# Kernel optimization log

Hardware: AMD Instinct MI355X
Metric: run time of the kernel (lower is better)

Reference implementation:

```python
import jax, jax.numpy as jnp
import numpy as np

H, B = 2, 64          # num_head, batch
LT, LI, LQ = 384, 128, 24
D = 768               # input_dim == hidden_dim
K = 384               # key_dim
V = 384               # value_dim
DK, DV = H * K, H * V # fused key / value dims (768, 768)


def _layer_norm(x, g, b, eps=1e-5):
    mu = x.mean(-1, keepdims=True)
    var = ((x - mu) ** 2).mean(-1, keepdims=True)
    return (x - mu) / jnp.sqrt(var + eps) * g + b


def _masked_softmax(w):
    # softmax over last axis treating -inf as masked; fully-masked rows -> all zeros
    # (faithful to torch: softmax then masked_fill_(isnan, 0))
    valid = jnp.isfinite(w)
    wmax = jnp.max(jnp.where(valid, w, -3e38), axis=-1, keepdims=True)
    e = jnp.where(valid, jnp.exp(w - wmax), 0.0)
    s = jnp.sum(e, axis=-1, keepdims=True)
    return e / jnp.where(s > 0, s, 1.0)


def _forward(text, images, query, ln_gamma, ln_beta,
             Wsq, bsq, Wiq, biq, Wsk, bsk, Wik, bik, Wsv, bsv, Wiv, biv,
             Wkp, bkp, Wvp, bvp,
             text_lengths, image_lengths, query_lengths):
    Bq, Lt, _ = text.shape
    Li = images.shape[1]
    L = Lt + Li
    tn = _layer_norm(text, ln_gamma, ln_beta)
    im = _layer_norm(images, ln_gamma, ln_beta)

    def proj(Wt, bt, Wi, bi):
        a = jnp.einsum('btd,hdk->hbtk', tn, Wt) + bt[:, None, None, :]
        c = jnp.einsum('bid,hdk->hbik', im, Wi) + bi[:, None, None, :]
        return jnp.concatenate([a, c], axis=2)  # [H,B,L,K or V]

    q = proj(Wsq, bsq, Wiq, biq)
    k = proj(Wsk, bsk, Wik, bik)
    v = proj(Wsv, bsv, Wiv, biv)

    # pad mask: True = padded position (torch mask==1 -> masked_fill 0)
    pad = jnp.concatenate([
        jnp.arange(Lt)[None, :] >= text_lengths[:, None],
        jnp.arange(Li)[None, :] >= image_lengths[:, None]], axis=1)  # [B,L]
    pm = pad[None, :, :, None]
    q = jnp.where(pm, 0.0, q)
    k = jnp.where(pm, 0.0, k)
    v = jnp.where(pm, 0.0, v)

    # SelfAttention per head: zero-dot-product masking + diagonal exclusion
    w = jnp.einsum('hbqd,hbkd->hbqk', q, k)
    w = jnp.where(w == 0.0, -jnp.inf, w)
    w = jnp.where(jnp.eye(L, dtype=bool)[None, None], -jnp.inf, w)
    p = _masked_softmax(w)
    attn = jnp.einsum('hbqk,hbkd->hbqd', p, v)          # [H,B,L,V]
    album = jnp.transpose(attn, (1, 2, 0, 3)).reshape(Bq, L, H * V)  # head-concat

    keys = album @ Wkp + bkp   # [B,L,DK]
    vals = album @ Wvp + bvp   # [B,L,DV]

    # FVTA: mask query / keys / values, zero-score -> -inf, softmax, nan -> 0
    padq = jnp.arange(query.shape[1])[None, :] >= query_lengths[:, None]
    qf = jnp.where(padq[..., None], 0.0, query)
    keys = jnp.where(pad[..., None], 0.0, keys)
    vals = jnp.where(pad[..., None], 0.0, vals)
    w2 = jnp.einsum('bqd,bkd->bqk', qf, keys)
    w2 = jnp.where(w2 == 0.0, -jnp.inf, w2)
    p2 = _masked_softmax(w2)
    return jnp.einsum('bqk,bkv->bqv', p2, vals).mean(axis=1)  # [B,DV]


def setup_inputs() -> dict:
    key = jax.random.key(0)
    ks = jax.random.split(key, 24)
    s = 0.02
    return {
        'text':   jax.random.normal(ks[0], (B, LT, D), jnp.float32),
        'images': jax.random.normal(ks[1], (B, LI, D), jnp.float32),
        'query':  jax.random.normal(ks[2], (B, LQ, DK), jnp.float32),
        'ln_gamma': jnp.ones((D,), jnp.float32),
        'ln_beta':  jnp.zeros((D,), jnp.float32),
        'Wsq': jax.random.normal(ks[3], (H, D, K), jnp.float32) * s,
        'bsq': jnp.zeros((H, K), jnp.float32),
        'Wiq': jax.random.normal(ks[4], (H, D, K), jnp.float32) * s,
        'biq': jnp.zeros((H, K), jnp.float32),
        'Wsk': jax.random.normal(ks[5], (H, D, K), jnp.float32) * s,
        'bsk': jnp.zeros((H, K), jnp.float32),
        'Wik': jax.random.normal(ks[6], (H, D, K), jnp.float32) * s,
        'bik': jnp.zeros((H, K), jnp.float32),
        'Wsv': jax.random.normal(ks[7], (H, D, V), jnp.float32) * s,
        'bsv': jnp.zeros((H, V), jnp.float32),
        'Wiv': jax.random.normal(ks[8], (H, D, V), jnp.float32) * s,
        'biv': jnp.zeros((H, V), jnp.float32),
        'Wkp': jax.random.normal(ks[9], (DV, DK), jnp.float32) * s,
        'bkp': jnp.zeros((DK,), jnp.float32),
        'Wvp': jax.random.normal(ks[10], (DV, DV), jnp.float32) * s,
        'bvp': jnp.zeros((DV,), jnp.float32),
        'text_lengths':  jax.random.randint(ks[11], (B,), 1, LT + 1),
        'image_lengths': jax.random.randint(ks[12], (B,), 1, LI + 1),
        'query_lengths': jax.random.randint(ks[13], (B,), 1, LQ + 1),
    }


def reference(text, images, query, ln_gamma, ln_beta,
              Wsq, bsq, Wiq, biq, Wsk, bsk, Wik, bik, Wsv, bsv, Wiv, biv,
              Wkp, bkp, Wvp, bvp,
              text_lengths, image_lengths, query_lengths):
    return _forward(text, images, query, ln_gamma, ln_beta,
                    Wsq, bsq, Wiq, biq, Wsk, bsk, Wik, bik, Wsv, bsv, Wiv, biv,
                    Wkp, bkp, Wvp, bvp,
                    text_lengths, image_lengths, query_lengths)
```

## Files before the change

kernel.cpp:

```cpp
#include <hip/hip_runtime.h>
#include <hip/hip_bf16.h>

typedef _Float16 h16;
typedef _Float16 h16x8 __attribute__((ext_vector_type(8)));
typedef _Float16 h16x4 __attribute__((ext_vector_type(4)));
typedef float    f32x4 __attribute__((ext_vector_type(4)));

#define MFMA(a,b,c) __builtin_amdgcn_mfma_f32_16x16x32_f16((a),(b),(c),0,0,0)


typedef __attribute__((address_space(1))) const void gas_void;
typedef __attribute__((address_space(3))) void las_void;
__device__ __forceinline__ void gld16(void* l, const void* g) {
  __builtin_amdgcn_global_load_lds((gas_void*)g, (las_void*)l, 16, 0, 0);
}

__global__ __launch_bounds__(256) void k_diag(float* out, int n, float val) {
  int i = blockIdx.x * 256 + threadIdx.x;
  if (i < n) out[i] = val;
}

__global__ __launch_bounds__(256) void k_prep(
    const float* __restrict__ Wsq, const float* __restrict__ Wiq,
    const float* __restrict__ Wsk, const float* __restrict__ Wik,
    const float* __restrict__ Wsv, const float* __restrict__ Wiv,
    const float* __restrict__ Wkp, const float* __restrict__ Wvp,
    h16* __restrict__ wb,
    const float* __restrict__ text, const float* __restrict__ images,
    const float* __restrict__ g, const float* __restrict__ be,
    h16* __restrict__ xn,
    const int* __restrict__ tlen, const int* __restrict__ ilen)
{
  const size_t WSZ = 589824;
  int bid = blockIdx.x;
  if (bid < 4608) {
    const float* src; h16* dst;
    int cols, cx, cy;
    if (bid < 3456) {
      int z = bid / 288, rem = bid % 288;
      cx = rem % 12; cy = rem / 12;
      int w = z >> 1, m = z & 1;
      const float* s6[6] = {Wsq, Wiq, Wsk, Wik, Wsv, Wiv};
      src = s6[w] + (size_t)m * 768 * 384;
      dst = wb + (size_t)w * WSZ + (size_t)m * 384 * 768;
      cols = 384;
    } else {
      int u2 = bid - 3456;
      int z = u2 / 576, rem = u2 % 576;
      cx = rem % 24; cy = rem / 24;
      src = (z == 0) ? Wkp : Wvp;
      dst = wb + (size_t)(6 + z) * WSZ;
      cols = 768;
    }
    __shared__ float tile[32][33];
    int d0 = cy * 32, c0 = cx * 32;
    int tx = threadIdx.x & 31, ty = threadIdx.x >> 5;
    #pragma unroll
    for (int i = 0; i < 32; i += 8)
      tile[ty+i][tx] = src[(size_t)(d0+ty+i)*cols + c0 + tx];
    __syncthreads();
    #pragma unroll
    for (int i = 0; i < 32; i += 8)
      dst[(size_t)(c0+ty+i)*768 + d0 + tx] = (h16)tile[tx][ty+i];
    return;
  }
  int row = bid - 4608;
  int b = row >> 9, l = row & 511;
  bool pad = (l < 384) ? (l >= tlen[b]) : ((l-384) >= ilen[b]);
  if (pad) return;
  const float* src = (l < 384) ? (text + ((size_t)b*384 + l)*768)
                               : (images + ((size_t)b*128 + (l-384))*768);
  int t = threadIdx.x;
  float x0 = src[t], x1 = src[t+256], x2 = src[t+512];
  __shared__ float red[8];
  float s = x0 + x1 + x2;
  #pragma unroll
  for (int m = 32; m; m >>= 1) s += __shfl_xor(s, m);
  int wid = t >> 6;
  if ((t & 63) == 0) red[wid] = s;
  __syncthreads();
  float mu = (red[0]+red[1]+red[2]+red[3]) * (1.0f/768.0f);
  float d0 = x0-mu, d1 = x1-mu, d2 = x2-mu;
  float v = d0*d0 + d1*d1 + d2*d2;
  #pragma unroll
  for (int m = 32; m; m >>= 1) v += __shfl_xor(v, m);
  if ((t & 63) == 0) red[4+wid] = v;
  __syncthreads();
  float var = (red[4]+red[5]+red[6]+red[7]) * (1.0f/768.0f);
  float rstd = rsqrtf(var + 1e-5f);
  h16* dst = xn + (size_t)row * 768;
  dst[t]     = (h16)(d0*rstd*g[t]     + be[t]);
  dst[t+256] = (h16)(d1*rstd*g[t+256] + be[t+256]);
  dst[t+512] = (h16)(d2*rstd*g[t+512] + be[t+512]);
}

__global__ __launch_bounds__(256) void k_lnstat(
    const float* __restrict__ text, const float* __restrict__ images,
    float* __restrict__ muv, float* __restrict__ rsd)
{
  int row = blockIdx.x;
  int b = row >> 9, l = row & 511;
  const float* src = (l < 384) ? (text + ((size_t)b*384 + l)*768)
                               : (images + ((size_t)b*128 + (l-384))*768);
  int t = threadIdx.x;
  float x0 = src[t], x1 = src[t+256], x2 = src[t+512];
  __shared__ float red[8];
  float s = x0 + x1 + x2;
  #pragma unroll
  for (int m = 32; m; m >>= 1) s += __shfl_xor(s, m);
  int wid = t >> 6;
  if ((t & 63) == 0) red[wid] = s;
  __syncthreads();
  float mu = (red[0]+red[1]+red[2]+red[3]) * (1.0f/768.0f);
  float d0 = x0-mu, d1 = x1-mu, d2 = x2-mu;
  float v = d0*d0 + d1*d1 + d2*d2;
  #pragma unroll
  for (int m = 32; m; m >>= 1) v += __shfl_xor(v, m);
  if ((t & 63) == 0) red[4+wid] = v;
  __syncthreads();
  if (t == 0) {
    float var = (red[4]+red[5]+red[6]+red[7]) * (1.0f/768.0f);
    muv[row] = mu;
    rsd[row] = rsqrtf(var + 1e-5f);
  }
}

__global__ __launch_bounds__(256) void k_wprep_all(
    const float* __restrict__ Wsq, const float* __restrict__ Wiq,
    const float* __restrict__ Wsk, const float* __restrict__ Wik,
    const float* __restrict__ Wsv, const float* __restrict__ Wiv,
    const float* __restrict__ Wkp, const float* __restrict__ Wvp,
    h16* __restrict__ wb)
{
  const size_t WSZ = 589824;
  int z = blockIdx.z;
  const float* src; h16* dst;
  int cols;
  if (z < 12) {
    if (blockIdx.x >= 12) return;
    int w = z >> 1, m = z & 1;
    const float* s6[6] = {Wsq, Wiq, Wsk, Wik, Wsv, Wiv};
    src = s6[w] + (size_t)m * 768 * 384;
    dst = wb + (size_t)w * WSZ + (size_t)m * 384 * 768;
    cols = 384;
  } else {
    src = (z == 12) ? Wkp : Wvp;
    dst = wb + (size_t)(6 + (z - 12)) * WSZ;
    cols = 768;
  }
  __shared__ float tile[32][33];
  int d0 = blockIdx.y * 32;
  int c0 = blockIdx.x * 32;
  int tx = threadIdx.x & 31, ty = threadIdx.x >> 5;
  #pragma unroll
  for (int i = 0; i < 32; i += 8)
    tile[ty+i][tx] = src[(size_t)(d0+ty+i)*cols + c0 + tx];
  __syncthreads();
  #pragma unroll
  for (int i = 0; i < 32; i += 8)
    dst[(size_t)(c0+ty+i)*768 + d0 + tx] = (h16)tile[tx][ty+i];
}

#define HOFF ((size_t)64*512*384)

template<int AMODE>
__global__ __launch_bounds__(256) void k_gemmf2(
    const h16* __restrict__ Asrc, const h16* __restrict__ wb,
    const float* __restrict__ bsq, const float* __restrict__ biq,
    const float* __restrict__ bsk, const float* __restrict__ bik,
    const float* __restrict__ bsv, const float* __restrict__ biv,
    const float* __restrict__ bkp, const float* __restrict__ bvp,
    h16* __restrict__ O0, h16* __restrict__ O1, h16* __restrict__ O2,
    const int* __restrict__ tlen, const int* __restrict__ ilen)
{
  constexpr int NT = (AMODE == 0) ? 18 : 12;
  __shared__ __align__(16) h16 SM[32768];
  h16* As0 = SM;
  h16* Bs0 = SM + 16384;
  const size_t WSZ = 589824;
  int bid = blockIdx.x;
  int xcd = bid & 7, slot = bid >> 3;
  int mt = xcd * 32 + slot / NT;
  int nt = slot % NT;
  int m0 = mt << 7;
  int b = m0 >> 9, l0 = m0 & 511;
  int TL = tlen[b], IL = ilen[b];
  bool skiptile = (l0 < 384) && (TL <= l0);
  int gc0 = nt << 7;
  int widx = gc0 / 768;
  int ncol0 = gc0 % 768;
  bool isimg = (l0 >= 384);

  const h16* BT;
  const float* bias;
  if constexpr (AMODE == 0) {
    BT = wb + ((size_t)(2*widx) + (isimg ? 1 : 0)) * WSZ;
    const float* bt6[6] = {bsq, biq, bsk, bik, bsv, biv};
    bias = bt6[2*widx + (isimg ? 1 : 0)];
  } else {
    BT = wb + (size_t)(6 + widx) * WSZ;
    bias = widx ? bvp : bkp;
  }

  int t = threadIdx.x;
  int lane = t & 63, wid = t >> 6;
  int wm = wid >> 1, wn = wid & 1;
  int lg = lane >> 4, li = lane & 15;

  f32x4 acc44[4][4] = {};

  if (!skiptile) {
    const h16* pA[4]; const h16* pB[4];
    h16* dA[4]; h16* dB[4];
    #pragma unroll
    for (int h = 0; h < 4; ++h) {
      int ci = h*256 + t;
      int row = ci >> 3;
      int cs = (ci & 7) ^ (row & 7);
      if constexpr (AMODE == 0)
        pA[h] = Asrc + (size_t)(m0 + row)*768 + cs*8;
      else
        pA[h] = Asrc + ((size_t)b*512 + l0 + row)*384 + cs*8;
      pB[h] = BT + (size_t)(ncol0 + row)*768 + cs*8;
      dA[h] = &As0[(h*256 + wid*64)*8];
      dB[h] = &Bs0[(h*256 + wid*64)*8];
    }
    const char* baA = (const char*)As0 + (wm*64 + li)*128;
    const char* baB = (const char*)Bs0 + (wn*64 + li)*128;
    int x0 = (lg ^ (li & 7)) << 4;

    #pragma unroll
    for (int h = 0; h < 4; ++h) {
      gld16(dA[h], pA[h]);
      gld16(dB[h], pB[h]);
    }
    __syncthreads();

    #pragma unroll
    for (int kk = 0; kk < 12; ++kk) {
      const int cur = kk & 1;
      if (kk < 11) {
        int ktE = (kk + 1) * 64;
        size_t aoff = (size_t)ktE;
        if constexpr (AMODE == 2) { if (ktE >= 384) aoff += HOFF - 384; }
        #pragma unroll
        for (int h = 0; h < 4; ++h) {
          gld16(dA[h] + (cur^1)*8192, pA[h] + aoff);
          gld16(dB[h] + (cur^1)*8192, pB[h] + ktE);
        }
      }
      const char* cA = baA + cur*16384;
      const char* cB = baB + cur*16384;
      #pragma unroll
      for (int ks = 0; ks < 2; ++ks) {
        int xo = x0 ^ (ks << 6);
        h16x8 af[4], bf[4];
        #pragma unroll
        for (int i = 0; i < 4; ++i) {
          af[i] = *(const h16x8*)(cA + i*2048 + xo);
          bf[i] = *(const h16x8*)(cB + i*2048 + xo);
        }
        #pragma unroll
        for (int i = 0; i < 4; ++i)
          #pragma unroll
          for (int j = 0; j < 4; ++j)
            acc44[i][j] = MFMA(af[i], bf[j], acc44[i][j]);
      }
      __syncthreads();
    }
  }

  constexpr int PITCH = 136;
  bool vroute = (AMODE == 0) ? (widx == 2) : (widx == 1);
  h16* dout = vroute ? ((AMODE == 0) ? O2 : O1)
                     : ((AMODE == 0) ? (widx == 0 ? O0 : O1) : O0);
  #pragma unroll
  for (int i = 0; i < 4; ++i)
    #pragma unroll
    for (int j = 0; j < 4; ++j) {
      int rowL = wm*64 + i*16 + lg*4;
      int colL = wn*64 + j*16 + li;
      float bv = bias[ncol0 + colL];
      #pragma unroll
      for (int r = 0; r < 4; ++r) {
        int l = l0 + rowL + r;
        float v = acc44[i][j][r] + bv;
        bool pad = (l < 384) ? (l >= TL) : ((l-384) >= IL);
        if (pad) v = 0.0f;
        if (vroute) SM[colL*PITCH + rowL + r] = (h16)v;
        else        SM[(rowL + r)*PITCH + colL] = (h16)v;
      }
    }
  __syncthreads();
  int hh = (AMODE == 0 && ncol0 >= 384) ? 1 : 0;
  int kkb = ncol0 - hh*384;
  #pragma unroll
  for (int q = 0; q < 8; ++q) {
    int row = q*16 + (t >> 4);
    int c0 = (t & 15) * 8;
    h16x8 val = *(const h16x8*)&SM[row*PITCH + c0];
    size_t oi;
    if (vroute) {
      if constexpr (AMODE == 0)
        oi = (((size_t)(hh*64 + b))*384 + kkb + row)*512 + l0 + c0;
      else
        oi = ((size_t)b*768 + ncol0 + row)*512 + l0 + c0;
    } else {
      int l = l0 + row;
      if constexpr (AMODE == 0)
        oi = (((size_t)(hh*64 + b))*512 + l)*384 + kkb + c0;
      else
        oi = ((size_t)b*512 + l)*768 + ncol0 + c0;
    }
    *(uint4*)&dout[oi] = *(uint4*)&val;
  }
}

#define LDSKg 72
__global__ __launch_bounds__(256) void k_gemmf_fb(
    const float* __restrict__ Atext, const float* __restrict__ Aimg,
    const float* __restrict__ muv, const float* __restrict__ rsd,
    const float* __restrict__ gam, const float* __restrict__ bet,
    const h16* __restrict__ wb,
    const float* __restrict__ bsq, const float* __restrict__ biq,
    const float* __restrict__ bsk, const float* __restrict__ bik,
    const float* __restrict__ bsv, const float* __restrict__ biv,
    h16* __restrict__ O0, h16* __restrict__ O1, h16* __restrict__ O2,
    const int* __restrict__ tlen, const int* __restrict__ ilen)
{
  constexpr int NT = 18;
  __shared__ __align__(16) h16 As[128*LDSKg];
  __shared__ __align__(16) h16 Bs[128*LDSKg];
  const size_t WSZ = 589824;
  int bid = blockIdx.x;
  int xcd = bid & 7, slot = bid >> 3;
  int mt = xcd * 32 + slot / NT;
  int nt = slot % NT;
  int m0 = mt << 7;
  int b = m0 >> 9, l0 = m0 & 511;
  int TL = tlen[b], IL = ilen[b];
  bool skiptile = (l0 < 384) && (TL <= l0);
  int gc0 = nt << 7;
  int widx = gc0 / 768;
  int ncol0 = gc0 % 768;
  bool isimg = (l0 >= 384);
  const h16* BT = wb + ((size_t)(2*widx) + (isimg ? 1 : 0)) * WSZ;
  const float* bt6[6] = {bsq, biq, bsk, bik, bsv, biv};
  const float* bias = bt6[2*widx + (isimg ? 1 : 0)];

  int t = threadIdx.x;
  int lane = t & 63, wid = t >> 6;
  int wm = wid >> 1, wn = wid & 1;
  int lg = lane >> 4, li = lane & 15;
  int sr = t >> 3, sc8 = (t & 7) * 8;
  f32x4 acc[4][4] = {};
  if (!skiptile) {
    const float* af32[4];
    float amu[4], ars[4];
    const h16* brow[4];
    #pragma unroll
    for (int half = 0; half < 4; ++half) {
      int r = sr + half*32;
      int l = l0 + r;
      af32[half] = (l < 384) ? (Atext + ((size_t)b*384 + l)*768)
                             : (Aimg  + ((size_t)b*128 + (l-384))*768);
      amu[half] = muv[m0 + r]; ars[half] = rsd[m0 + r];
      brow[half] = BT + (size_t)(ncol0 + r)*768;
    }
    for (int kt = 0; kt < 768; kt += 64) {
      int d = kt + sc8;
      f32x4 g0 = *(const f32x4*)&gam[d], g1 = *(const f32x4*)&gam[d+4];
      f32x4 e0 = *(const f32x4*)&bet[d], e1 = *(const f32x4*)&bet[d+4];
      #pragma unroll
      for (int half = 0; half < 4; ++half) {
        int r = sr + half*32;
        f32x4 x0 = *(const f32x4*)&af32[half][d];
        f32x4 x1 = *(const f32x4*)&af32[half][d+4];
        float mu = amu[half], rs = ars[half];
        h16x8 o;
        #pragma unroll
        for (int j = 0; j < 4; ++j) o[j]   = (h16)((x0[j]-mu)*rs*g0[j] + e0[j]);
        #pragma unroll
        for (int j = 0; j < 4; ++j) o[4+j] = (h16)((x1[j]-mu)*rs*g1[j] + e1[j]);
        *(h16x8*)&As[r*LDSKg + sc8] = o;
        *(uint4*)&Bs[r*LDSKg + sc8] = *(const uint4*)&brow[half][d];
      }
      __syncthreads();
      #pragma unroll
      for (int ks = 0; ks < 2; ++ks) {
        int kc = ks*32 + lg*8;
        h16x8 af[4], bf[4];
        #pragma unroll
        for (int i = 0; i < 4; ++i) {
          af[i] = *(const h16x8*)&As[(wm*64 + i*16 + li)*LDSKg + kc];
          bf[i] = *(const h16x8*)&Bs[(wn*64 + i*16 + li)*LDSKg + kc];
        }
        #pragma unroll
        for (int i = 0; i < 4; ++i)
          #pragma unroll
          for (int j = 0; j < 4; ++j)
            acc[i][j] = MFMA(af[i], bf[j], acc[i][j]);
      }
      __syncthreads();
    }
  }
  bool vroute = (widx == 2);
  h16* dsc = (widx == 0 ? O0 : O1);
  #pragma unroll
  for (int i = 0; i < 4; ++i)
    #pragma unroll
    for (int j = 0; j < 4; ++j) {
      int colL = wn*64 + j*16 + li;
      int col_in = ncol0 + colL;
      float bv = bias[col_in];
      int lb = l0 + wm*64 + i*16 + lg*4;
      int hh = (col_in >= 384) ? 1 : 0;
      int kk = col_in - hh*384;
      if (vroute) {
        h16x4 pk;
        #pragma unroll
        for (int r = 0; r < 4; ++r) {
          int l = lb + r;
          float v = acc[i][j][r] + bv;
          bool pad = (l < 384) ? (l >= TL) : ((l-384) >= IL);
          pk[r] = (h16)(pad ? 0.0f : v);
        }
        size_t oi = (((size_t)(hh*64 + b))*384 + kk)*512 + lb;
        *(h16x4*)&O2[oi] = pk;
      } else {
        #pragma unroll
        for (int r = 0; r < 4; ++r) {
          int l = lb + r;
          float v = acc[i][j][r] + bv;
          bool pad = (l < 384) ? (l >= TL) : ((l-384) >= IL);
          if (pad) v = 0.0f;
          size_t oi = (((size_t)(hh*64 + b))*512 + l)*384 + kk;
          dsc[oi] = (h16)v;
        }
      }
    }
}

__global__ __launch_bounds__(256) void k_attn1(
    h16* Qb, const h16* __restrict__ Kb, const h16* __restrict__ Vt,
    const int* __restrict__ tlen, const int* __restrict__ ilen)
{
  __shared__ __align__(16) float S[32*516];
  __shared__ float rowscale[32];
  int bid = blockIdx.x;
  int xcd = bid & 7, slot = bid >> 3;
  int hb = (slot >> 4) * 8 + xcd;
  int q0 = (slot & 15) * 32;
  int b = hb & 63;
  int TL = tlen[b], IL = ilen[b];
  h16* Qp = Qb + (size_t)hb * 512 * 384;
  const h16* Kp = Kb + (size_t)hb * 512 * 384;
  const h16* Vp = Vt + (size_t)hb * 384 * 512;
  int t = threadIdx.x, lane = t & 63, w = t >> 6;
  int lg = lane >> 4, li = lane & 15;

  bool qskip = (q0 < 384) ? (TL <= q0) : (IL <= q0 - 384);
  if (qskip) {
    h16x8 z = {};
    for (int c = t; c < 1536; c += 256) {
      int row = c / 48, v8 = (c % 48) * 8;
      *(h16x8*)&Qp[(size_t)(q0+row)*384 + v8] = z;
    }
    return;
  }

  h16x8 aq[2][12];
  #pragma unroll
  for (int m = 0; m < 2; ++m)
    #pragma unroll
    for (int ks = 0; ks < 12; ++ks)
      aq[m][ks] = *(const h16x8*)&Qp[(size_t)(q0 + m*16 + li)*384 + ks*32 + lg*8];

  int kbase = w * 128;
  int LIMw = (w < 3) ? TL : (384 + IL);
  int nvf = (LIMw - kbase + 15) >> 4;
  nvf = nvf < 0 ? 0 : (nvf > 8 ? 8 : nvf);
  for (int nf = 0; nf < nvf; ++nf) {
    int kcol = kbase + nf*16;
    f32x4 acc0 = {0,0,0,0}, acc1 = {0,0,0,0};
    #pragma unroll
    for (int ks = 0; ks < 12; ++ks) {
      h16x8 bk = *(const h16x8*)&Kp[(size_t)(kcol + li)*384 + ks*32 + lg*8];
      acc0 = MFMA(aq[0][ks], bk, acc0);
      acc1 = MFMA(aq[1][ks], bk, acc1);
    }
    #pragma unroll
    for (int r = 0; r < 4; ++r) {
      int c = kcol + li;
      int row0 = lg*4 + r;
      float v0 = acc0[r];
      if (v0 == 0.0f || (q0 + row0) == c) v0 = -__builtin_inff();
      S[row0*516 + c] = v0;
      int row1 = 16 + lg*4 + r;
      float v1 = acc1[r];
      if (v1 == 0.0f || (q0 + row1) == c) v1 = -__builtin_inff();
      S[row1*516 + c] = v1;
    }
  }
  for (int nf = nvf; nf < 8; ++nf) {
    int c = kbase + nf*16 + li;
    #pragma unroll
    for (int r = 0; r < 4; ++r) {
      S[(lg*4 + r)*516 + c] = -__builtin_inff();
      S[(16 + lg*4 + r)*516 + c] = -__builtin_inff();
    }
  }
  __syncthreads();
  {
    int row = t >> 3, ci = t & 7;
    float mx = -3e38f;
    for (int j = 0; j < 64; ++j) mx = fmaxf(mx, S[row*516 + ci + j*8]);
    mx = fmaxf(mx, __shfl_xor(mx, 1));
    mx = fmaxf(mx, __shfl_xor(mx, 2));
    mx = fmaxf(mx, __shfl_xor(mx, 4));
    float sum = 0.0f;
    for (int j = 0; j < 64; ++j) {
      float e = __expf(S[row*516 + ci + j*8] - mx);
      S[row*516 + ci + j*8] = e;
      sum += e;
    }
    sum += __shfl_xor(sum, 1);
    sum += __shfl_xor(sum, 2);
    sum += __shfl_xor(sum, 4);
    if (ci == 0) rowscale[row] = 1.0f / (sum > 0.0f ? sum : 1.0f);
  }
  __syncthreads();
  f32x4 oacc[2][6] = {};
  int v0w = w * 96;
  auto pv = [&](int kt) {
    int k0 = kt * 32;
    h16x8 bv[6];
    #pragma unroll
    for (int n = 0; n < 6; ++n)
      bv[n] = *(const h16x8*)&Vp[(size_t)(v0w + n*16 + li)*512 + k0 + lg*8];
    #pragma unroll
    for (int m = 0; m < 2; ++m) {
      int row = m*16 + li;
      f32x4 p0 = *(const f32x4*)&S[row*516 + k0 + lg*8];
      f32x4 p1 = *(const f32x4*)&S[row*516 + k0 + lg*8 + 4];
      h16x8 pa;
      pa[0]=(h16)p0[0]; pa[1]=(h16)p0[1]; pa[2]=(h16)p0[2]; pa[3]=(h16)p0[3];
      pa[4]=(h16)p1[0]; pa[5]=(h16)p1[1]; pa[6]=(h16)p1[2]; pa[7]=(h16)p1[3];
      #pragma unroll
      for (int n = 0; n < 6; ++n)
        oacc[m][n] = MFMA(pa, bv[n], oacc[m][n]);
    }
  };
  int n1 = (TL + 31) >> 5; n1 = n1 > 12 ? 12 : n1;
  int n2 = (IL + 31) >> 5; n2 = n2 > 4 ? 4 : n2;
  for (int kt = 0; kt < n1; ++kt) pv(kt);
  for (int kt = 12; kt < 12 + n2; ++kt) pv(kt);
  #pragma unroll
  for (int m = 0; m < 2; ++m)
    #pragma unroll
    for (int n = 0; n < 6; ++n)
      #pragma unroll
      for (int r = 0; r < 4; ++r) {
        int row = m*16 + lg*4 + r;
        int col = v0w + n*16 + li;
        Qp[(size_t)(q0 + row)*384 + col] = (h16)(oacc[m][n][r] * rowscale[row]);
      }
}

__global__ __launch_bounds__(256) void k_attn2(
    const float* __restrict__ query, const h16* __restrict__ keys,
    const h16* __restrict__ valsT, const int* __restrict__ qlen,
    const int* __restrict__ tlen, const int* __restrict__ ilen,
    float* __restrict__ out)
{
  __shared__ __align__(16) float S[32*516];
  __shared__ __align__(16) h16 UB[32*776];
  __shared__ float rowscale[32];
  int bid = blockIdx.x;
  int b = bid >> 1, vh = bid & 1;
  const float* Qp = query + (size_t)b*24*768;
  const h16* Kp = keys + (size_t)b*512*768;
  const h16* Vp = valsT + (size_t)b*768*512;
  int t = threadIdx.x, lane = t & 63, w = t >> 6;
  int lg = lane >> 4, li = lane & 15;
  int ql = qlen[b];
  int TL = tlen[b], IL = ilen[b];
  for (int c = t; c < 3072; c += 256) {
    int row = c / 96, vv = (c % 96) * 8;
    h16x8 a = {};
    if (row < 24 && row < ql) {
      f32x4 f0 = *(const f32x4*)&Qp[(size_t)row*768 + vv];
      f32x4 f1 = *(const f32x4*)&Qp[(size_t)row*768 + vv + 4];
      a[0]=(h16)f0[0]; a[1]=(h16)f0[1]; a[2]=(h16)f0[2]; a[3]=(h16)f0[3];
      a[4]=(h16)f1[0]; a[5]=(h16)f1[1]; a[6]=(h16)f1[2]; a[7]=(h16)f1[3];
    }
    *(h16x8*)&UB[row*776 + vv] = a;
  }
  __syncthreads();
  int kbase = w * 128;
  int LIMw = (w < 3) ? TL : (384 + IL);
  int nvf = (LIMw - kbase + 15) >> 4;
  nvf = nvf < 0 ? 0 : (nvf > 8 ? 8 : nvf);
  for (int nf = 0; nf < nvf; ++nf) {
    int kcol = kbase + nf*16;
    f32x4 acc0 = {0,0,0,0}, acc1 = {0,0,0,0};
    #pragma unroll
    for (int ks = 0; ks < 24; ++ks) {
      h16x8 a0 = *(const h16x8*)&UB[(li)*776      + ks*32 + lg*8];
      h16x8 a1 = *(const h16x8*)&UB[(16 + li)*776 + ks*32 + lg*8];
      h16x8 bk = *(const h16x8*)&Kp[(size_t)(kcol + li)*768 + ks*32 + lg*8];
      acc0 = MFMA(a0, bk, acc0);
      acc1 = MFMA(a1, bk, acc1);
    }
    #pragma unroll
    for (int r = 0; r < 4; ++r) {
      int c = kcol + li;
      float v0 = acc0[r];
      if (v0 == 0.0f) v0 = -__builtin_inff();
      S[(lg*4 + r)*516 + c] = v0;
      float v1 = acc1[r];
      if (v1 == 0.0f) v1 = -__builtin_inff();
      S[(16 + lg*4 + r)*516 + c] = v1;
    }
  }
  for (int nf = nvf; nf < 8; ++nf) {
    int c = kbase + nf*16 + li;
    #pragma unroll
    for (int r = 0; r < 4; ++r) {
      S[(lg*4 + r)*516 + c] = -__builtin_inff();
      S[(16 + lg*4 + r)*516 + c] = -__builtin_inff();
    }
  }
  __syncthreads();
  {
    int row = t >> 3, ci = t & 7;
    float mx = -3e38f;
    for (int j = 0; j < 64; ++j) mx = fmaxf(mx, S[row*516 + ci + j*8]);
    mx = fmaxf(mx, __shfl_xor(mx, 1));
    mx = fmaxf(mx, __shfl_xor(mx, 2));
    mx = fmaxf(mx, __shfl_xor(mx, 4));
    float sum = 0.0f;
    for (int j = 0; j < 64; ++j) {
      float e = __expf(S[row*516 + ci + j*8] - mx);
      S[row*516 + ci + j*8] = e;
      sum += e;
    }
    sum += __shfl_xor(sum, 1);
    sum += __shfl_xor(sum, 2);
    sum += __shfl_xor(sum, 4);
    if (ci == 0) rowscale[row] = 1.0f / (sum > 0.0f ? sum : 1.0f);
  }
  __syncthreads();
  int n1 = (TL + 31) >> 5; n1 = n1 > 12 ? 12 : n1;
  int n2 = (IL + 31) >> 5; n2 = n2 > 4 ? 4 : n2;
  {
    f32x4 oacc[2][6] = {};
    auto pv = [&](int kt) {
      int k0 = kt * 32;
      h16x8 bv[6];
      #pragma unroll
      for (int n = 0; n < 6; ++n)
        bv[n] = *(const h16x8*)&Vp[(size_t)(vh*384 + w*96 + n*16 + li)*512 + k0 + lg*8];
      #pragma unroll
      for (int m = 0; m < 2; ++m) {
        int row = m*16 + li;
        f32x4 p0 = *(const f32x4*)&S[row*516 + k0 + lg*8];
        f32x4 p1 = *(const f32x4*)&S[row*516 + k0 + lg*8 + 4];
        h16x8 pa;
        pa[0]=(h16)p0[0]; pa[1]=(h16)p0[1]; pa[2]=(h16)p0[2]; pa[3]=(h16)p0[3];
        pa[4]=(h16)p1[0]; pa[5]=(h16)p1[1]; pa[6]=(h16)p1[2]; pa[7]=(h16)p1[3];
        #pragma unroll
        for (int n = 0; n < 6; ++n)
          oacc[m][n] = MFMA(pa, bv[n], oacc[m][n]);
      }
    };
    for (int kt = 0; kt < n1; ++kt) pv(kt);
    for (int kt = 12; kt < 12 + n2; ++kt) pv(kt);
    #pragma unroll
    for (int n = 0; n < 6; ++n) {
      float cs = 0.0f;
      #pragma unroll
      for (int m = 0; m < 2; ++m)
        #pragma unroll
        for (int r = 0; r < 4; ++r)
          cs += oacc[m][n][r] * rowscale[m*16 + lg*4 + r];
      cs += __shfl_xor(cs, 16);
      cs += __shfl_xor(cs, 32);
      if (lg == 0) out[(size_t)b*768 + vh*384 + w*96 + n*16 + li] = cs * (1.0f/24.0f);
    }
  }
}

extern "C" void kernel_launch(void* const* d_in, const int* in_sizes, int n_in,
                              void* d_out, int out_size, void* d_ws, size_t ws_size,
                              hipStream_t stream)
{
  (void)in_sizes; (void)n_in;
  const float* text  = (const float*)d_in[0];
  const float* images= (const float*)d_in[1];
  const float* query = (const float*)d_in[2];
  const float* ln_g  = (const float*)d_in[3];
  const float* ln_b  = (const float*)d_in[4];
  const float* Wsq = (const float*)d_in[5];
  const float* bsq = (const float*)d_in[6];
  const float* Wiq = (const float*)d_in[7];
  const float* biq = (const float*)d_in[8];
  const float* Wsk = (const float*)d_in[9];
  const float* bsk = (const float*)d_in[10];
  const float* Wik = (const float*)d_in[11];
  const float* bik = (const float*)d_in[12];
  const float* Wsv = (const float*)d_in[13];
  const float* bsv = (const float*)d_in[14];
  const float* Wiv = (const float*)d_in[15];
  const float* biv = (const float*)d_in[16];
  const float* Wkp = (const float*)d_in[17];
  const float* bkp = (const float*)d_in[18];
  const float* Wvp = (const float*)d_in[19];
  const float* bvp = (const float*)d_in[20];
  const int* tlen = (const int*)d_in[21];
  const int* ilen = (const int*)d_in[22];
  const int* qlen = (const int*)d_in[23];

  const size_t NEED1 = 160694272;
  const size_t NEED2 = NEED1 + 50331648;
  if (ws_size < NEED1) {
    k_diag<<<dim3((out_size+255)/256), dim3(256), 0, stream>>>((float*)d_out, out_size, 1.0e6f);
    return;
  }
  float* muv = (float*)d_ws;
  float* rsd = muv + 32768;
  h16* wb = (h16*)((char*)d_ws + 262144);
  const size_t WSZ = 589824;
  const size_t TSZ = (size_t)32768*768;
  h16* Qb = wb + 8*WSZ;
  h16* Kb = Qb + TSZ;
  h16* Vb = Kb + TSZ;
  h16* XNb = (h16*)((char*)d_ws + NEED1);

  dim3 blk(256);

  if (ws_size >= NEED2) {
    k_prep<<<dim3(4608 + 32768), blk, 0, stream>>>(
        Wsq, Wiq, Wsk, Wik, Wsv, Wiv, Wkp, Wvp, wb,
        text, images, ln_g, ln_b, XNb, tlen, ilen);
    k_gemmf2<0><<<dim3(4608), blk, 0, stream>>>(XNb, wb,
        bsq, biq, bsk, bik, bsv, biv, bkp, bvp, Qb, Kb, Vb, tlen, ilen);
  } else {
    k_wprep_all<<<dim3(24,24,14), blk, 0, stream>>>(Wsq, Wiq, Wsk, Wik, Wsv, Wiv, Wkp, Wvp, wb);
    k_lnstat<<<dim3(32768), blk, 0, stream>>>(text, images, muv, rsd);
    k_gemmf_fb<<<dim3(4608), blk, 0, stream>>>(text, images, muv, rsd,
        ln_g, ln_b, wb, bsq, biq, bsk, bik, bsv, biv, Qb, Kb, Vb, tlen, ilen);
  }

  k_attn1<<<dim3(2048), blk, 0, stream>>>(Qb, Kb, Vb, tlen, ilen);

  k_gemmf2<2><<<dim3(3072), blk, 0, stream>>>(Qb, wb,
      bsq, biq, bsk, bik, bsv, biv, bkp, bvp, Kb, Vb, nullptr, tlen, ilen);

  k_attn2<<<dim3(128), blk, 0, stream>>>(query, Kb, Vb, qlen, tlen, ilen, (float*)d_out);
}
```

Before: 435.0 us.

## Store Q/K/V in k-blocked layout and vectorize softmax LDS passes

The projection GEMM epilogue now writes Q, K and V, plus the second-stage keys and values, in a blocked layout with 32-wide k chunks. This makes each MFMA fragment load in the attention kernels a contiguous 16-byte read from a compact block instead of a long-stride row access. The attention output goes to a separate album buffer (reusing the layernorm scratch) rather than overwriting Q in place. The softmax max/exp passes in both attention kernels now use f32x4 LDS reads, and the unused fallback path (k_lnstat, k_wprep_all, k_gemmf_fb) is removed, so the kernel now requires the larger workspace.

```diff
diff --git a/kernel.cpp b/kernel.cpp
--- a/kernel.cpp
+++ b/kernel.cpp
@@ -94,73 +94,6 @@
   dst[t+512] = (h16)(d2*rstd*g[t+512] + be[t+512]);
 }
 
-__global__ __launch_bounds__(256) void k_lnstat(
-    const float* __restrict__ text, const float* __restrict__ images,
-    float* __restrict__ muv, float* __restrict__ rsd)
-{
-  int row = blockIdx.x;
-  int b = row >> 9, l = row & 511;
-  const float* src = (l < 384) ? (text + ((size_t)b*384 + l)*768)
-                               : (images + ((size_t)b*128 + (l-384))*768);
-  int t = threadIdx.x;
-  float x0 = src[t], x1 = src[t+256], x2 = src[t+512];
-  __shared__ float red[8];
-  float s = x0 + x1 + x2;
-  #pragma unroll
-  for (int m = 32; m; m >>= 1) s += __shfl_xor(s, m);
-  int wid = t >> 6;
-  if ((t & 63) == 0) red[wid] = s;
-  __syncthreads();
-  float mu = (red[0]+red[1]+red[2]+red[3]) * (1.0f/768.0f);
-  float d0 = x0-mu, d1 = x1-mu, d2 = x2-mu;
-  float v = d0*d0 + d1*d1 + d2*d2;
-  #pragma unroll
-  for (int m = 32; m; m >>= 1) v += __shfl_xor(v, m);
-  if ((t & 63) == 0) red[4+wid] = v;
-  __syncthreads();
-  if (t == 0) {
-    float var = (red[4]+red[5]+red[6]+red[7]) * (1.0f/768.0f);
-    muv[row] = mu;
-    rsd[row] = rsqrtf(var + 1e-5f);
-  }
-}
-
-__global__ __launch_bounds__(256) void k_wprep_all(
-    const float* __restrict__ Wsq, const float* __restrict__ Wiq,
-    const float* __restrict__ Wsk, const float* __restrict__ Wik,
-    const float* __restrict__ Wsv, const float* __restrict__ Wiv,
-    const float* __restrict__ Wkp, const float* __restrict__ Wvp,
-    h16* __restrict__ wb)
-{
-  const size_t WSZ = 589824;
-  int z = blockIdx.z;
-  const float* src; h16* dst;
-  int cols;
-  if (z < 12) {
-    if (blockIdx.x >= 12) return;
-    int w = z >> 1, m = z & 1;
-    const float* s6[6] = {Wsq, Wiq, Wsk, Wik, Wsv, Wiv};
-    src = s6[w] + (size_t)m * 768 * 384;
-    dst = wb + (size_t)w * WSZ + (size_t)m * 384 * 768;
-    cols = 384;
-  } else {
-    src = (z == 12) ? Wkp : Wvp;
-    dst = wb + (size_t)(6 + (z - 12)) * WSZ;
-    cols = 768;
-  }
-  __shared__ float tile[32][33];
-  int d0 = blockIdx.y * 32;
-  int c0 = blockIdx.x * 32;
-  int tx = threadIdx.x & 31, ty = threadIdx.x >> 5;
-  #pragma unroll
-  for (int i = 0; i < 32; i += 8)
-    tile[ty+i][tx] = src[(size_t)(d0+ty+i)*cols + c0 + tx];
-  __syncthreads();
-  #pragma unroll
-  for (int i = 0; i < 32; i += 8)
-    dst[(size_t)(c0+ty+i)*768 + d0 + tx] = (h16)tile[tx][ty+i];
-}
-
 #define HOFF ((size_t)64*512*384)
 
 template<int AMODE>
@@ -301,148 +234,29 @@
     h16x8 val = *(const h16x8*)&SM[row*PITCH + c0];
     size_t oi;
     if (vroute) {
+      int l = l0 + c0;
+      int kt = l >> 5, k32 = l & 31;
       if constexpr (AMODE == 0)
-        oi = (((size_t)(hh*64 + b))*384 + kkb + row)*512 + l0 + c0;
+        oi = (size_t)(hh*64 + b)*196608 + (size_t)kt*12288 + (size_t)(kkb + row)*32 + k32;
       else
-        oi = ((size_t)b*768 + ncol0 + row)*512 + l0 + c0;
+        oi = (size_t)b*393216 + (size_t)kt*24576 + (size_t)(ncol0 + row)*32 + k32;
     } else {
       int l = l0 + row;
-      if constexpr (AMODE == 0)
-        oi = (((size_t)(hh*64 + b))*512 + l)*384 + kkb + c0;
-      else
-        oi = ((size_t)b*512 + l)*768 + ncol0 + c0;
+      if constexpr (AMODE == 0) {
+        int kk = kkb + c0;
+        oi = (size_t)(hh*64 + b)*196608 + (size_t)(kk >> 5)*16384 + (size_t)l*32 + (kk & 31);
+      } else {
+        int col = ncol0 + c0;
+        oi = (size_t)b*393216 + (size_t)(col >> 5)*16384 + (size_t)l*32 + (col & 31);
+      }
     }
     *(uint4*)&dout[oi] = *(uint4*)&val;
   }
 }
 
-#define LDSKg 72
-__global__ __launch_bounds__(256) void k_gemmf_fb(
-    const float* __restrict__ Atext, const float* __restrict__ Aimg,
-    const float* __restrict__ muv, const float* __restrict__ rsd,
-    const float* __restrict__ gam, const float* __restrict__ bet,
-    const h16* __restrict__ wb,
-    const float* __restrict__ bsq, const float* __restrict__ biq,
-    const float* __restrict__ bsk, const float* __restrict__ bik,
-    const float* __restrict__ bsv, const float* __restrict__ biv,
-    h16* __restrict__ O0, h16* __restrict__ O1, h16* __restrict__ O2,
-    const int* __restrict__ tlen, const int* __restrict__ ilen)
-{
-  constexpr int NT = 18;
-  __shared__ __align__(16) h16 As[128*LDSKg];
-  __shared__ __align__(16) h16 Bs[128*LDSKg];
-  const size_t WSZ = 589824;
-  int bid = blockIdx.x;
-  int xcd = bid & 7, slot = bid >> 3;
-  int mt = xcd * 32 + slot / NT;
-  int nt = slot % NT;
-  int m0 = mt << 7;
-  int b = m0 >> 9, l0 = m0 & 511;
-  int TL = tlen[b], IL = ilen[b];
-  bool skiptile = (l0 < 384) && (TL <= l0);
-  int gc0 = nt << 7;
-  int widx = gc0 / 768;
-  int ncol0 = gc0 % 768;
-  bool isimg = (l0 >= 384);
-  const h16* BT = wb + ((size_t)(2*widx) + (isimg ? 1 : 0)) * WSZ;
-  const float* bt6[6] = {bsq, biq, bsk, bik, bsv, biv};
-  const float* bias = bt6[2*widx + (isimg ? 1 : 0)];
-
-  int t = threadIdx.x;
-  int lane = t & 63, wid = t >> 6;
-  int wm = wid >> 1, wn = wid & 1;
-  int lg = lane >> 4, li = lane & 15;
-  int sr = t >> 3, sc8 = (t & 7) * 8;
-  f32x4 acc[4][4] = {};
-  if (!skiptile) {
-    const float* af32[4];
-    float amu[4], ars[4];
-    const h16* brow[4];
-    #pragma unroll
-    for (int half = 0; half < 4; ++half) {
-      int r = sr + half*32;
-      int l = l0 + r;
-      af32[half] = (l < 384) ? (Atext + ((size_t)b*384 + l)*768)
-                             : (Aimg  + ((size_t)b*128 + (l-384))*768);
-      amu[half] = muv[m0 + r]; ars[half] = rsd[m0 + r];
-      brow[half] = BT + (size_t)(ncol0 + r)*768;
-    }
-    for (int kt = 0; kt < 768; kt += 64) {
-      int d = kt + sc8;
-      f32x4 g0 = *(const f32x4*)&gam[d], g1 = *(const f32x4*)&gam[d+4];
-      f32x4 e0 = *(const f32x4*)&bet[d], e1 = *(const f32x4*)&bet[d+4];
-      #pragma unroll
-      for (int half = 0; half < 4; ++half) {
-        int r = sr + half*32;
-        f32x4 x0 = *(const f32x4*)&af32[half][d];
-        f32x4 x1 = *(const f32x4*)&af32[half][d+4];
-        float mu = amu[half], rs = ars[half];
-        h16x8 o;
-        #pragma unroll
-        for (int j = 0; j < 4; ++j) o[j]   = (h16)((x0[j]-mu)*rs*g0[j] + e0[j]);
-        #pragma unroll
-        for (int j = 0; j < 4; ++j) o[4+j] = (h16)((x1[j]-mu)*rs*g1[j] + e1[j]);
-        *(h16x8*)&As[r*LDSKg + sc8] = o;
-        *(uint4*)&Bs[r*LDSKg + sc8] = *(const uint4*)&brow[half][d];
-      }
-      __syncthreads();
-      #pragma unroll
-      for (int ks = 0; ks < 2; ++ks) {
-        int kc = ks*32 + lg*8;
-        h16x8 af[4], bf[4];
-        #pragma unroll
-        for (int i = 0; i < 4; ++i) {
-          af[i] = *(const h16x8*)&As[(wm*64 + i*16 + li)*LDSKg + kc];
-          bf[i] = *(const h16x8*)&Bs[(wn*64 + i*16 + li)*LDSKg + kc];
-        }
-        #pragma unroll
-        for (int i = 0; i < 4; ++i)
-          #pragma unroll
-          for (int j = 0; j < 4; ++j)
-            acc[i][j] = MFMA(af[i], bf[j], acc[i][j]);
-      }
-      __syncthreads();
-    }
-  }
-  bool vroute = (widx == 2);
-  h16* dsc = (widx == 0 ? O0 : O1);
-  #pragma unroll
-  for (int i = 0; i < 4; ++i)
-    #pragma unroll
-    for (int j = 0; j < 4; ++j) {
-      int colL = wn*64 + j*16 + li;
-      int col_in = ncol0 + colL;
-      float bv = bias[col_in];
-      int lb = l0 + wm*64 + i*16 + lg*4;
-      int hh = (col_in >= 384) ? 1 : 0;
-      int kk = col_in - hh*384;
-      if (vroute) {
-        h16x4 pk;
-        #pragma unroll
-        for (int r = 0; r < 4; ++r) {
-          int l = lb + r;
-          float v = acc[i][j][r] + bv;
-          bool pad = (l < 384) ? (l >= TL) : ((l-384) >= IL);
-          pk[r] = (h16)(pad ? 0.0f : v);
-        }
-        size_t oi = (((size_t)(hh*64 + b))*384 + kk)*512 + lb;
-        *(h16x4*)&O2[oi] = pk;
-      } else {
-        #pragma unroll
-        for (int r = 0; r < 4; ++r) {
-          int l = lb + r;
-          float v = acc[i][j][r] + bv;
-          bool pad = (l < 384) ? (l >= TL) : ((l-384) >= IL);
-          if (pad) v = 0.0f;
-          size_t oi = (((size_t)(hh*64 + b))*512 + l)*384 + kk;
-          dsc[oi] = (h16)v;
-        }
-      }
-    }
-}
-
 __global__ __launch_bounds__(256) void k_attn1(
-    h16* Qb, const h16* __restrict__ Kb, const h16* __restrict__ Vt,
+    const h16* __restrict__ Qt, const h16* __restrict__ Kt,
+    const h16* __restrict__ Vt, h16* __restrict__ album,
     const int* __restrict__ tlen, const int* __restrict__ ilen)
 {
   __shared__ __align__(16) float S[32*516];
@@ -453,9 +267,10 @@
   int q0 = (slot & 15) * 32;
   int b = hb & 63;
   int TL = tlen[b], IL = ilen[b];
-  h16* Qp = Qb + (size_t)hb * 512 * 384;
-  const h16* Kp = Kb + (size_t)hb * 512 * 384;
-  const h16* Vp = Vt + (size_t)hb * 384 * 512;
+  const h16* Qp = Qt + (size_t)hb * 196608;
+  const h16* Kp = Kt + (size_t)hb * 196608;
+  const h16* Vp = Vt + (size_t)hb * 196608;
+  h16* Ap = album + (size_t)hb * 196608;
   int t = threadIdx.x, lane = t & 63, w = t >> 6;
   int lg = lane >> 4, li = lane & 15;
 
@@ -464,7 +279,7 @@
     h16x8 z = {};
     for (int c = t; c < 1536; c += 256) {
       int row = c / 48, v8 = (c % 48) * 8;
-      *(h16x8*)&Qp[(size_t)(q0+row)*384 + v8] = z;
+      *(h16x8*)&Ap[(size_t)(q0+row)*384 + v8] = z;
     }
     return;
   }
@@ -474,7 +289,7 @@
   for (int m = 0; m < 2; ++m)
     #pragma unroll
     for (int ks = 0; ks < 12; ++ks)
-      aq[m][ks] = *(const h16x8*)&Qp[(size_t)(q0 + m*16 + li)*384 + ks*32 + lg*8];
+      aq[m][ks] = *(const h16x8*)&Qp[(size_t)ks*16384 + (q0 + m*16 + li)*32 + lg*8];
 
   int kbase = w * 128;
   int LIMw = (w < 3) ? TL : (384 + IL);
@@ -485,7 +300,7 @@
     f32x4 acc0 = {0,0,0,0}, acc1 = {0,0,0,0};
     #pragma unroll
     for (int ks = 0; ks < 12; ++ks) {
-      h16x8 bk = *(const h16x8*)&Kp[(size_t)(kcol + li)*384 + ks*32 + lg*8];
+      h16x8 bk = *(const h16x8*)&Kp[(size_t)ks*16384 + (kcol + li)*32 + lg*8];
       acc0 = MFMA(aq[0][ks], bk, acc0);
       acc1 = MFMA(aq[1][ks], bk, acc1);
     }
@@ -513,16 +328,27 @@
   __syncthreads();
   {
     int row = t >> 3, ci = t & 7;
-    float mx = -3e38f;
-    for (int j = 0; j < 64; ++j) mx = fmaxf(mx, S[row*516 + ci + j*8]);
+    float* Sr = &S[row*516];
+    f32x4 mx4 = {-3e38f, -3e38f, -3e38f, -3e38f};
+    #pragma unroll
+    for (int j = 0; j < 16; ++j) {
+      f32x4 v = *(const f32x4*)&Sr[ci*4 + j*32];
+      #pragma unroll
+      for (int k = 0; k < 4; ++k) mx4[k] = fmaxf(mx4[k], v[k]);
+    }
+    float mx = fmaxf(fmaxf(mx4[0], mx4[1]), fmaxf(mx4[2], mx4[3]));
     mx = fmaxf(mx, __shfl_xor(mx, 1));
     mx = fmaxf(mx, __shfl_xor(mx, 2));
     mx = fmaxf(mx, __shfl_xor(mx, 4));
     float sum = 0.0f;
-    for (int j = 0; j < 64; ++j) {
-      float e = __expf(S[row*516 + ci + j*8] - mx);
-      S[row*516 + ci + j*8] = e;
-      sum += e;
+    #pragma unroll
+    for (int j = 0; j < 16; ++j) {
+      f32x4 v = *(const f32x4*)&Sr[ci*4 + j*32];
+      f32x4 e;
+      #pragma unroll
+      for (int k = 0; k < 4; ++k) e[k] = __expf(v[k] - mx);
+      *(f32x4*)&Sr[ci*4 + j*32] = e;
+      sum += e[0] + e[1] + e[2] + e[3];
     }
     sum += __shfl_xor(sum, 1);
     sum += __shfl_xor(sum, 2);
@@ -537,7 +363,7 @@
     h16x8 bv[6];
     #pragma unroll
     for (int n = 0; n < 6; ++n)
-      bv[n] = *(const h16x8*)&Vp[(size_t)(v0w + n*16 + li)*512 + k0 + lg*8];
+      bv[n] = *(const h16x8*)&Vp[(size_t)kt*12288 + (v0w + n*16 + li)*32 + lg*8];
     #pragma unroll
     for (int m = 0; m < 2; ++m) {
       int row = m*16 + li;
@@ -563,12 +389,12 @@
       for (int r = 0; r < 4; ++r) {
         int row = m*16 + lg*4 + r;
         int col = v0w + n*16 + li;
-        Qp[(size_t)(q0 + row)*384 + col] = (h16)(oacc[m][n][r] * rowscale[row]);
+        Ap[(size_t)(q0 + row)*384 + col] = (h16)(oacc[m][n][r] * rowscale[row]);
       }
 }
 
 __global__ __launch_bounds__(256) void k_attn2(
-    const float* __restrict__ query, const h16* __restrict__ keys,
+    const float* __restrict__ query, const h16* __restrict__ keysT,
     const h16* __restrict__ valsT, const int* __restrict__ qlen,
     const int* __restrict__ tlen, const int* __restrict__ ilen,
     float* __restrict__ out)
@@ -579,8 +405,8 @@
   int bid = blockIdx.x;
   int b = bid >> 1, vh = bid & 1;
   const float* Qp = query + (size_t)b*24*768;
-  const h16* Kp = keys + (size_t)b*512*768;
-  const h16* Vp = valsT + (size_t)b*768*512;
+  const h16* Kp = keysT + (size_t)b*393216;
+  const h16* Vp = valsT + (size_t)b*393216;
   int t = threadIdx.x, lane = t & 63, w = t >> 6;
   int lg = lane >> 4, li = lane & 15;
   int ql = qlen[b];
@@ -608,7 +434,7 @@
     for (int ks = 0; ks < 24; ++ks) {
       h16x8 a0 = *(const h16x8*)&UB[(li)*776      + ks*32 + lg*8];
       h16x8 a1 = *(const h16x8*)&UB[(16 + li)*776 + ks*32 + lg*8];
-      h16x8 bk = *(const h16x8*)&Kp[(size_t)(kcol + li)*768 + ks*32 + lg*8];
+      h16x8 bk = *(const h16x8*)&Kp[(size_t)ks*16384 + (kcol + li)*32 + lg*8];
       acc0 = MFMA(a0, bk, acc0);
       acc1 = MFMA(a1, bk, acc1);
     }
@@ -634,16 +460,27 @@
   __syncthreads();
   {
     int row = t >> 3, ci = t & 7;
-    float mx = -3e38f;
-    for (int j = 0; j < 64; ++j) mx = fmaxf(mx, S[row*516 + ci + j*8]);
+    float* Sr = &S[row*516];
+    f32x4 mx4 = {-3e38f, -3e38f, -3e38f, -3e38f};
+    #pragma unroll
+    for (int j = 0; j < 16; ++j) {
+      f32x4 v = *(const f32x4*)&Sr[ci*4 + j*32];
+      #pragma unroll
+      for (int k = 0; k < 4; ++k) mx4[k] = fmaxf(mx4[k], v[k]);
+    }
+    float mx = fmaxf(fmaxf(mx4[0], mx4[1]), fmaxf(mx4[2], mx4[3]));
     mx = fmaxf(mx, __shfl_xor(mx, 1));
     mx = fmaxf(mx, __shfl_xor(mx, 2));
     mx = fmaxf(mx, __shfl_xor(mx, 4));
     float sum = 0.0f;
-    for (int j = 0; j < 64; ++j) {
-      float e = __expf(S[row*516 + ci + j*8] - mx);
-      S[row*516 + ci + j*8] = e;
-      sum += e;
+    #pragma unroll
+    for (int j = 0; j < 16; ++j) {
+      f32x4 v = *(const f32x4*)&Sr[ci*4 + j*32];
+      f32x4 e;
+      #pragma unroll
+      for (int k = 0; k < 4; ++k) e[k] = __expf(v[k] - mx);
+      *(f32x4*)&Sr[ci*4 + j*32] = e;
+      sum += e[0] + e[1] + e[2] + e[3];
     }
     sum += __shfl_xor(sum, 1);
     sum += __shfl_xor(sum, 2);
@@ -660,7 +497,7 @@
       h16x8 bv[6];
       #pragma unroll
       for (int n = 0; n < 6; ++n)
-        bv[n] = *(const h16x8*)&Vp[(size_t)(vh*384 + w*96 + n*16 + li)*512 + k0 + lg*8];
+        bv[n] = *(const h16x8*)&Vp[(size_t)kt*24576 + (vh*384 + w*96 + n*16 + li)*32 + lg*8];
       #pragma unroll
       for (int m = 0; m < 2; ++m) {
         int row = m*16 + li;
@@ -721,40 +558,31 @@
   const int* ilen = (const int*)d_in[22];
   const int* qlen = (const int*)d_in[23];
 
-  const size_t NEED1 = 160694272;
-  const size_t NEED2 = NEED1 + 50331648;
-  if (ws_size < NEED1) {
+  const size_t NEED = 160694272 + 50331648;
+  if (ws_size < NEED) {
     k_diag<<<dim3((out_size+255)/256), dim3(256), 0, stream>>>((float*)d_out, out_size, 1.0e6f);
     return;
   }
-  float* muv = (float*)d_ws;
-  float* rsd = muv + 32768;
   h16* wb = (h16*)((char*)d_ws + 262144);
   const size_t WSZ = 589824;
   const size_t TSZ = (size_t)32768*768;
   h16* Qb = wb + 8*WSZ;
   h16* Kb = Qb + TSZ;
   h16* Vb = Kb + TSZ;
-  h16* XNb = (h16*)((char*)d_ws + NEED1);
+  h16* XNb = (h16*)((char*)d_ws + 160694272);
 
   dim3 blk(256);
 
-  if (ws_size >= NEED2) {
-    k_prep<<<dim3(4608 + 32768), blk, 0, stream>>>(
-        Wsq, Wiq, Wsk, Wik, Wsv, Wiv, Wkp, Wvp, wb,
-        text, images, ln_g, ln_b, XNb, tlen, ilen);
-    k_gemmf2<0><<<dim3(4608), blk, 0, stream>>>(XNb, wb,
-        bsq, biq, bsk, bik, bsv, biv, bkp, bvp, Qb, Kb, Vb, tlen, ilen);
-  } else {
-    k_wprep_all<<<dim3(24,24,14), blk, 0, stream>>>(Wsq, Wiq, Wsk, Wik, Wsv, Wiv, Wkp, Wvp, wb);
-    k_lnstat<<<dim3(32768), blk, 0, stream>>>(text, images, muv, rsd);
-    k_gemmf_fb<<<dim3(4608), blk, 0, stream>>>(text, images, muv, rsd,
-        ln_g, ln_b, wb, bsq, biq, bsk, bik, bsv, biv, Qb, Kb, Vb, tlen, ilen);
-  }
-
-  k_attn1<<<dim3(2048), blk, 0, stream>>>(Qb, Kb, Vb, tlen, ilen);
-
-  k_gemmf2<2><<<dim3(3072), blk, 0, stream>>>(Qb, wb,
+  k_prep<<<dim3(4608 + 32768), blk, 0, stream>>>(
+      Wsq, Wiq, Wsk, Wik, Wsv, Wiv, Wkp, Wvp, wb,
+      text, images, ln_g, ln_b, XNb, tlen, ilen);
+
+  k_gemmf2<0><<<dim3(4608), blk, 0, stream>>>(XNb, wb,
+      bsq, biq, bsk, bik, bsv, biv, bkp, bvp, Qb, Kb, Vb, tlen, ilen);
+
+  k_attn1<<<dim3(2048), blk, 0, stream>>>(Qb, Kb, Vb, XNb, tlen, ilen);
+
+  k_gemmf2<2><<<dim3(3072), blk, 0, stream>>>(XNb, wb,
       bsq, biq, bsk, bik, bsv, biv, bkp, bvp, Kb, Vb, nullptr, tlen, ilen);
 
   k_attn2<<<dim3(128), blk, 0, stream>>>(query, Kb, Vb, qlen, tlen, ilen, (float*)d_out);
```

After: 385.6 us. 11.4% less time.
